# Kernel tuning notes

Measured on AMD Instinct MI355X. Metric: run time of the kernel, lower is better.

## Reference

```python
import jax, jax.numpy as jnp
import numpy as np

MS0 = 4            # base sector size (ms[0])
MS1 = 4            # top sector size (r=[1] -> ms[-1]=ms0)
Q = 2              # q_length (Ising spin states)
C = 512            # c_length
LAYERS = 2
B = 256
L = 16
FS = MS0 * MS0 - 1  # neighborhood size, excludes target pixel


def setup_inputs():
    key = jax.random.key(0)
    ks = jax.random.split(key, 8)
    v = jax.random.randint(ks[0], (B, L, L), 0, Q, dtype=jnp.int32)
    u = v.astype(jnp.float32)
    emb = jax.random.normal(ks[1], (FS, Q, C), dtype=jnp.float32)  # fs embedding tables

    def lin_w(k, out_d, in_d):
        b = 1.0 / np.sqrt(in_d)
        return jax.random.uniform(k, (out_d, in_d), minval=-b, maxval=b, dtype=jnp.float32)

    def lin_b(k, out_d, in_d):
        b = 1.0 / np.sqrt(in_d)
        return jax.random.uniform(k, (out_d,), minval=-b, maxval=b, dtype=jnp.float32)

    k2a, k2b = jax.random.split(ks[2])
    k3a, k3b = jax.random.split(ks[3])
    mlp_w1 = lin_w(k2a, C, C)
    mlp_b1 = lin_b(k2b, C, C)
    mlp_w2 = lin_w(k3a, Q, C)
    mlp_b2 = lin_b(k3b, Q, C)

    def lstm_p(k, in_d):
        k1, k2, k3, k4 = jax.random.split(k, 4)
        b = 1.0 / np.sqrt(C)
        wi = jax.random.uniform(k1, (4 * C, in_d), minval=-b, maxval=b, dtype=jnp.float32)
        wh = jax.random.uniform(k2, (4 * C, C), minval=-b, maxval=b, dtype=jnp.float32)
        bi = jax.random.uniform(k3, (4 * C,), minval=-b, maxval=b, dtype=jnp.float32)
        bh = jax.random.uniform(k4, (4 * C,), minval=-b, maxval=b, dtype=jnp.float32)
        return wi, wh, bi, bh

    w_ih0, w_hh0, b_ih0, b_hh0 = lstm_p(ks[4], MS1 * MS1)
    w_ih1, w_hh1, b_ih1, b_hh1 = lstm_p(ks[5], C)
    return dict(u=u, v=v, emb=emb,
                mlp_w1=mlp_w1, mlp_b1=mlp_b1, mlp_w2=mlp_w2, mlp_b2=mlp_b2,
                w_ih0=w_ih0, w_hh0=w_hh0, b_ih0=b_ih0, b_hh0=b_hh0,
                w_ih1=w_ih1, w_hh1=w_hh1, b_ih1=b_ih1, b_hh1=b_hh1)


def _forward(u, v, emb, mlp_w1, mlp_b1, mlp_w2, mlp_b2,
             w_ih0, w_hh0, b_ih0, b_hh0, w_ih1, w_hh1, b_ih1, b_hh1):
    n_sec = L // MS0
    margin = MS0 - 1
    lstm_params = ((w_ih0, w_hh0, b_ih0, b_hh0), (w_ih1, w_hh1, b_ih1, b_hh1))

    def lstm_step(x, state):
        # single-timestep multi-layer LSTM (eval mode, no dropout)
        h, c = state  # [LAYERS, B, C] each
        hs, cs = [], []
        inp = x
        for l, (wi, wh, bi, bh) in enumerate(lstm_params):
            g = inp @ wi.T + bi + h[l] @ wh.T + bh
            gi, gf, gg, go = jnp.split(g, 4, axis=-1)  # torch gate order i,f,g,o
            cn = jax.nn.sigmoid(gf) * c[l] + jax.nn.sigmoid(gi) * jnp.tanh(gg)
            hn = jax.nn.sigmoid(go) * jnp.tanh(cn)
            hs.append(hn)
            cs.append(cn)
            inp = hn
        return (jnp.stack(hs), jnp.stack(cs))

    zeros_state = lambda: (jnp.zeros((LAYERS, B, C), jnp.float32),
                           jnp.zeros((LAYERS, B, C), jnp.float32))
    memi = [zeros_state() for _ in range(n_sec)]
    memj = [zeros_state() for _ in range(n_sec)]
    sector = [0, 0]
    softout = jnp.zeros((B, L, L, Q), jnp.float32)
    nbr = jnp.arange(FS)[None, :]  # [1, FS] embedding-table indices
    key = jax.random.key(1234)

    for i in range(n_sec - 1):
        for j in range(n_sec - 1):
            si, sj = i * MS0, j * MS0
            ns0, ns1 = MS1 * (si // MS1), MS1 * (sj // MS1)
            if ns1 != sector[1]:
                sector = [ns0, ns1]
                for s in range(n_sec):
                    uv = u[:, s * MS1:(s + 1) * MS1, sector[1]:sector[1] + MS1].reshape(B, MS1 * MS1)
                    memj[s] = lstm_step(uv, memj[s])
            if ns0 != sector[0]:
                sector[0] = ns0
                uv = u[:, sector[0] - MS1:sector[0], sector[1]:sector[1] + MS1].reshape(B, MS1 * MS1)
                memi[sector[0] // MS1] = lstm_step(uv, memi[sector[0] // MS1])
            h0 = memj[i][0][0] + memi[j][0][0]  # layer-0 hidden sum, [B, C]
            for ii in range(MS0):
                for jj in range(MS0):
                    a, b = si + ii + 1, sj + jj + 1
                    pr, pc = a + margin, b + margin  # target pixel (bottom-right of patch)
                    patch = v[:, a:a + MS0, b:b + MS0].reshape(B, MS0 * MS0)[:, :FS]  # mask drops (margin,margin)
                    xemb = emb[nbr, patch, :].sum(axis=1)  # [B, C]
                    z = jax.nn.relu((xemb + h0) @ mlp_w1.T + mlp_b1)
                    logits = jax.nn.log_softmax(z @ mlp_w2.T + mlp_b2, axis=-1)  # [B, Q]
                    softout = softout.at[:, pr, pc].set(logits)
                    key, sub = jax.random.split(key)
                    samp = jax.random.categorical(sub, logits, axis=-1)  # [B]
                    v = v.at[:, pr, pc].set(samp.astype(v.dtype))
                    u = u.at[:, pr, pc].set(samp.astype(u.dtype))
    return softout, u, v


def reference(u, v, emb, mlp_w1, mlp_b1, mlp_w2, mlp_b2,
              w_ih0, w_hh0, b_ih0, b_hh0, w_ih1, w_hh1, b_ih1, b_hh1):
    return _forward(u, v, emb, mlp_w1, mlp_b1, mlp_w2, mlp_b2,
                    w_ih0, w_hh0, b_ih0, b_hh0, w_ih1, w_hh1, b_ih1, b_hh1)
```

## Files before the change

kernel.cpp:

```cpp
#include <hip/hip_runtime.h>
#include <cstdint>
#include <cstddef>

constexpr int NB = 256;
constexpr int NC = 512;
constexpr int NL = 16;
constexpr int NFS = 15;

#define PARTITIONABLE 1

struct TFOut { uint32_t a, b; };

__host__ __device__ constexpr uint32_t rotl32(uint32_t x, int d) {
  return (x << d) | (x >> (32 - d));
}

__host__ __device__ constexpr TFOut tf2x32(uint32_t k0, uint32_t k1,
                                           uint32_t x0, uint32_t x1) {
  uint32_t k2 = k0 ^ k1 ^ 0x1BD11BDAu;
  x0 += k0; x1 += k1;
  const int R0[4] = {13, 15, 26, 6};
  const int R1[4] = {17, 29, 16, 24};
  for (int i = 0; i < 4; i++) { x0 += x1; x1 = rotl32(x1, R0[i]); x1 ^= x0; }
  x0 += k1; x1 += k2 + 1u;
  for (int i = 0; i < 4; i++) { x0 += x1; x1 = rotl32(x1, R1[i]); x1 ^= x0; }
  x0 += k2; x1 += k0 + 2u;
  for (int i = 0; i < 4; i++) { x0 += x1; x1 = rotl32(x1, R0[i]); x1 ^= x0; }
  x0 += k0; x1 += k1 + 3u;
  for (int i = 0; i < 4; i++) { x0 += x1; x1 = rotl32(x1, R1[i]); x1 ^= x0; }
  x0 += k1; x1 += k2 + 4u;
  for (int i = 0; i < 4; i++) { x0 += x1; x1 = rotl32(x1, R0[i]); x1 ^= x0; }
  x0 += k2; x1 += k0 + 5u;
  return TFOut{x0, x1};
}

struct SubKeys { uint32_t v[288]; };

constexpr SubKeys make_subkeys() {
  SubKeys s{};
  uint32_t k0 = 0u, k1 = 1234u;
  for (int t = 0; t < 144; t++) {
#if PARTITIONABLE
    TFOut nk = tf2x32(k0, k1, 0u, 0u);
    TFOut sk = tf2x32(k0, k1, 0u, 1u);
    s.v[2 * t] = sk.a; s.v[2 * t + 1] = sk.b;
    k0 = nk.a; k1 = nk.b;
#else
    TFOut p0 = tf2x32(k0, k1, 0u, 2u);
    TFOut p1 = tf2x32(k0, k1, 1u, 3u);
    s.v[2 * t] = p0.b; s.v[2 * t + 1] = p1.b;
    k0 = p0.a; k1 = p1.a;
#endif
  }
  return s;
}

__constant__ SubKeys SUBKEYS = make_subkeys();

__device__ __forceinline__ float gumbel_from_bits(uint32_t bits) {
  uint32_t ub = (bits >> 9) | 0x3f800000u;
  float f = __uint_as_float(ub) - 1.0f;
  float u = (f == 0.0f) ? 1.17549435e-38f : f;
  float inner = logf(u);
  float outer = logf(-inner);
  return -outer;
}

typedef __attribute__((ext_vector_type(8))) short bf16x8;
typedef __attribute__((ext_vector_type(4))) float f32x4;

__device__ __forceinline__ void gl2lds16(const unsigned short* g,
                                         unsigned short* l) {
  __builtin_amdgcn_global_load_lds(
      (const __attribute__((address_space(1))) unsigned int*)g,
      (__attribute__((address_space(3))) unsigned int*)l, 16, 0, 0);
}

__device__ __forceinline__ uint32_t bf_rne(float x) {
  uint32_t u = __float_as_uint(x);
  return (u + 0x7fffu + ((u >> 16) & 1u)) >> 16;
}

__global__ __launch_bounds__(256) void setup_kernel(
    const float* __restrict__ u_in, const int* __restrict__ v_in,
    float* __restrict__ h0buf, float* __restrict__ cbuf,
    float* __restrict__ u_cur, int* __restrict__ v_cur,
    float* __restrict__ out_soft, float* __restrict__ out_u,
    float* __restrict__ out_v, unsigned int* __restrict__ az) {
  int idx = blockIdx.x * 256 + threadIdx.x;
  if (idx < 786432) h0buf[idx] = 0.0f;
  if (idx < 3 * NB * NC) cbuf[idx] = 0.0f;
  if (idx < 786432) az[idx] = 0u;
  if (idx < NB * NL * NL) {
    float uv = u_in[idx];
    int vv = v_in[idx];
    u_cur[idx] = uv;
    v_cur[idx] = vv;
    out_u[idx] = uv;
    out_v[idx] = (float)vv;
  }
  if (idx < NB * NL * NL * 2) out_soft[idx] = 0.0f;
}

__global__ __launch_bounds__(256) void split_w_kernel(
    const float* __restrict__ whh,
    unsigned short* __restrict__ Bhi, unsigned short* __restrict__ Blo) {
  int idx = blockIdx.x * 256 + threadIdx.x;
  float x = whh[idx];
  uint32_t hb = bf_rne(x);
  float lo = x - __uint_as_float(hb << 16);
  Bhi[idx] = (unsigned short)hb;
  Blo[idx] = (unsigned short)bf_rne(lo);
}

__global__ __launch_bounds__(256) void wd_kernel(
    const float* __restrict__ emb, const float* __restrict__ w1,
    const float* __restrict__ b1, float* __restrict__ WD,
    float* __restrict__ A0v) {
  __shared__ double dvec[NC];
  int n = blockIdx.x, tid = threadIdx.x;
  for (int k = tid; k < NC; k += 256) {
    if (n < NFS) {
      dvec[k] = (double)emb[(n * 2 + 1) * NC + k] - (double)emb[(n * 2) * NC + k];
    } else {
      double s = 0.0;
      for (int nn = 0; nn < NFS; nn++) s += (double)emb[(nn * 2) * NC + k];
      dvec[k] = s;
    }
  }
  __syncthreads();
  for (int c = tid; c < NC; c += 256) {
    double acc = 0.0;
    const float* wrow = w1 + (size_t)c * NC;
    for (int k = 0; k < NC; k++) acc += dvec[k] * (double)wrow[k];
    if (n < NFS) WD[n * NC + c] = (float)acc;
    else         A0v[c] = (float)(acc + (double)b1[c]);
  }
}

__global__ __launch_bounds__(256) void lstm_fused2_kernel(
    const unsigned short* __restrict__ Ah_r, const unsigned short* __restrict__ Al_r,
    unsigned short* __restrict__ Ah_w, unsigned short* __restrict__ Al_w,
    const unsigned short* __restrict__ Bhi, const unsigned short* __restrict__ Blo,
    const float* __restrict__ wih, const float* __restrict__ u_cur,
    const float* __restrict__ bih, const float* __restrict__ bhh,
    float* __restrict__ cbuf, float* __restrict__ h_out, int col0) {
  __shared__ __align__(16) unsigned short SM[24576];
  __shared__ float uvs[32][16];

  unsigned short* sA  = SM;
  unsigned short* sAl = SM + 4096;
  unsigned short* sB  = SM + 8192;
  unsigned short* sBl = SM + 16384;

  int bx0 = blockIdx.x;
  int xcd = bx0 & 7;
  int i5 = bx0 >> 3;
  int ct = xcd * 4 + (i5 & 3);
  int rt = i5 >> 2;
  int tid = threadIdx.x;
  int w = tid >> 6, lane = tid & 63;
  int l15 = lane & 15, kg = lane >> 4;
  int sw = (l15 >> 1) & 3;
  int grow0 = rt * 32;
  int s = rt >> 3;
  int b0 = (rt & 7) * 32;

  {
    int idx = tid;
    for (int t = 0; t < 2; t++, idx += 256) {
      int r = idx >> 4, nn = idx & 15;
      uvs[r][nn] =
          u_cur[(b0 + r) * 256 + (s * 4 + (nn >> 2)) * 16 + col0 + (nn & 3)];
    }
  }

  f32x4 acc[2][4];
#pragma unroll
  for (int i = 0; i < 2; i++)
#pragma unroll
    for (int j = 0; j < 4; j++) acc[i][j] = (f32x4){0.f, 0.f, 0.f, 0.f};

  for (int kc = 0; kc < 4; kc++) {
    int k0 = w * 128 + kc * 32;
    if (kc > 0) __syncthreads();
#pragma unroll
    for (int q = 0; q < 2; q++) {
      int slot = q * 64 + lane;
      int r = slot >> 2;
      int c2 = (slot & 3) ^ ((r >> 1) & 3);
      size_t so = (size_t)(grow0 + r) * 512 + k0 + c2 * 8;
      gl2lds16(Ah_r + so, sA + w * 1024 + q * 512);
      gl2lds16(Al_r + so, sAl + w * 1024 + q * 512);
    }
#pragma unroll
    for (int q = 0; q < 4; q++) {
      int slot = q * 64 + lane;
      int r = slot >> 2;
      int c2 = (slot & 3) ^ ((r >> 1) & 3);
      int nidx = (r >> 4) * 512 + ct * 16 + (r & 15);
      size_t so = (size_t)nidx * 512 + k0 + c2 * 8;
      gl2lds16(Bhi + so, sB + w * 2048 + q * 512);
      gl2lds16(Blo + so, sBl + w * 2048 + q * 512);
    }
    __syncthreads();

    bf16x8 ah[2], al[2];
#pragma unroll
    for (int i = 0; i < 2; i++) {
      int ro = w * 1024 + (i * 16 + l15) * 32 + ((kg ^ sw) * 8);
      ah[i] = *(const bf16x8*)&sA[ro];
      al[i] = *(const bf16x8*)&sAl[ro];
    }
#pragma unroll
    for (int j = 0; j < 4; j++) {
      int ro = w * 2048 + (j * 16 + l15) * 32 + ((kg ^ sw) * 8);
      bf16x8 bh = *(const bf16x8*)&sB[ro];
      bf16x8 bl = *(const bf16x8*)&sBl[ro];
#pragma unroll
      for (int i = 0; i < 2; i++) {
        acc[i][j] = __builtin_amdgcn_mfma_f32_16x16x32_bf16(ah[i], bh,
                                                            acc[i][j], 0, 0, 0);
        acc[i][j] = __builtin_amdgcn_mfma_f32_16x16x32_bf16(ah[i], bl,
                                                            acc[i][j], 0, 0, 0);
        acc[i][j] = __builtin_amdgcn_mfma_f32_16x16x32_bf16(al[i], bh,
                                                            acc[i][j], 0, 0, 0);
      }
    }
  }

  float* red = (float*)SM;
  __syncthreads();
#pragma unroll
  for (int i = 0; i < 2; i++)
#pragma unroll
    for (int g = 0; g < 4; g++)
#pragma unroll
      for (int rr = 0; rr < 4; rr++) {
        int row = i * 16 + kg * 4 + rr;
        red[((w * 4 + g) * 32 + row) * 17 + l15] = acc[i][g][rr];
      }
  __syncthreads();

  int rbase = tid >> 4, c = tid & 15;
  int cglob = ct * 16 + c;
  float bi_[4], bh_[4];
#pragma unroll
  for (int g = 0; g < 4; g++) {
    bi_[g] = bih[g * 512 + cglob];
    bh_[g] = bhh[g * 512 + cglob];
  }
#pragma unroll
  for (int rh = 0; rh < 2; rh++) {
    int row = rh * 16 + rbase;
    int grow = grow0 + row;
    float uvr[16];
#pragma unroll
    for (int nn = 0; nn < 16; nn++) uvr[nn] = uvs[row][nn];
    float gv[4];
#pragma unroll
    for (int g = 0; g < 4; g++) {
      float v = 0.0f;
#pragma unroll
      for (int ww = 0; ww < 4; ww++)
        v += red[((ww * 4 + g) * 32 + row) * 17 + c];
      const float* wr = wih + (size_t)(g * 512 + cglob) * 16;
#pragma unroll
      for (int nn = 0; nn < 16; nn++) v = fmaf(uvr[nn], wr[nn], v);
      gv[g] = v + bi_[g] + bh_[g];
    }
    size_t off = (size_t)grow * NC + cglob;
    float c_old = cbuf[off];
    float sig_i = 1.0f / (1.0f + expf(-gv[0]));
    float sig_f = 1.0f / (1.0f + expf(-gv[1]));
    float tg    = tanhf(gv[2]);
    float sig_o = 1.0f / (1.0f + expf(-gv[3]));
    float cn = sig_f * c_old + sig_i * tg;
    float hn = sig_o * tanhf(cn);
    cbuf[off] = cn;
    h_out[off] = hn;
    uint32_t hb = bf_rne(hn);
    float lo = hn - __uint_as_float(hb << 16);
    Ah_w[off] = (unsigned short)hb;
    Al_w[off] = (unsigned short)bf_rne(lo);
  }
}

__global__ __launch_bounds__(256) void w1h0_kernel(
    const float* __restrict__ h_in,
    const float* __restrict__ w1, float* __restrict__ Hpart) {
  int bx = blockIdx.x;
  int ks = bx >> 5;
  int bt = (bx >> 3) & 3;
  int ct = bx & 7;
  int tid = threadIdx.x, tn = tid & 15, tb = tid >> 4;

  __shared__ float hs[64][36];
  __shared__ float wt[64][36];
  float acc[4][4] = {};
  const float* hbase = h_in + (size_t)(bt * 64) * NC;

  for (int kc = 0; kc < 2; kc++) {
    int k0 = ks * 64 + kc * 32;
    __syncthreads();
    for (int t = 0; t < 2; t++) {
      int idx = tid + t * 256;
      int row = idx >> 3, kk4 = idx & 7;
      *(float4*)&hs[row][kk4 * 4] =
          *(const float4*)(hbase + (size_t)row * NC + k0 + kk4 * 4);
      int wrow = ct * 64 + row;
      *(float4*)&wt[row][kk4 * 4] =
          *(const float4*)(w1 + (size_t)wrow * NC + k0 + kk4 * 4);
    }
    __syncthreads();
#pragma unroll
    for (int kk4 = 0; kk4 < 8; kk4++) {
      float4 hv[4], wv[4];
#pragma unroll
      for (int i = 0; i < 4; i++) hv[i] = *(float4*)&hs[tb * 4 + i][kk4 * 4];
#pragma unroll
      for (int j = 0; j < 4; j++) wv[j] = *(float4*)&wt[tn + 16 * j][kk4 * 4];
#pragma unroll
      for (int i = 0; i < 4; i++)
#pragma unroll
        for (int j = 0; j < 4; j++)
          acc[i][j] += hv[i].x * wv[j].x + hv[i].y * wv[j].y +
                       hv[i].z * wv[j].z + hv[i].w * wv[j].w;
    }
  }
#pragma unroll
  for (int i = 0; i < 4; i++) {
    int b = bt * 64 + tb * 4 + i;
#pragma unroll
    for (int j = 0; j < 4; j++) {
      int cidx = ct * 64 + tn + 16 * j;
      Hpart[((size_t)ks * NB + b) * NC + cidx] = acc[i][j];
    }
  }
}

__global__ __launch_bounds__(64) void pixel_kernel(
    const float* __restrict__ WD, const float* __restrict__ A0v,
    const float* __restrict__ Hpart, const float* __restrict__ w2,
    const float* __restrict__ b2, float* __restrict__ u_cur,
    int* __restrict__ v_cur, float* __restrict__ out_soft,
    float* __restrict__ out_u, float* __restrict__ out_v,
    int si, int sj, int t_base) {
  int b = blockIdx.x, lane = threadIdx.x;
  __shared__ float gum[32];

  int widx = (lane < 49) ? lane : 48;
  int vv = v_cur[b * 256 + (si + 1 + widx / 7) * 16 + (sj + 1 + widx % 7)];
  unsigned long long mask = __ballot((lane < 49) && (vv != 0));

  if (lane < 32) {
    int t = t_base + (lane >> 1);
    uint32_t sk0 = SUBKEYS.v[2 * t], sk1 = SUBKEYS.v[2 * t + 1];
    uint32_t bits;
#if PARTITIONABLE
    TFOut o = tf2x32(sk0, sk1, 0u, (uint32_t)(2 * b + (lane & 1)));
    bits = o.a ^ o.b;
#else
    uint32_t f = (uint32_t)(2 * b + (lane & 1));
    if (f < 256u) { TFOut o = tf2x32(sk0, sk1, f, f + 256u); bits = o.a; }
    else          { TFOut o = tf2x32(sk0, sk1, f - 256u, f); bits = o.b; }
#endif
    gum[lane] = gumbel_from_bits(bits);
  }

  float wdreg[NFS][8];
#pragma unroll
  for (int n = 0; n < NFS; n++)
#pragma unroll
    for (int r = 0; r < 8; r++) wdreg[n][r] = WD[n * NC + lane + 64 * r];

  float w2r0[8], w2r1[8];
#pragma unroll
  for (int r = 0; r < 8; r++) {
    w2r0[r] = w2[lane + 64 * r];
    w2r1[r] = w2[NC + lane + 64 * r];
  }
  double b20 = (double)b2[0], b21 = (double)b2[1];

  float base[8];
#pragma unroll
  for (int r = 0; r < 8; r++) {
    int c = lane + 64 * r;
    float v = A0v[c];
#pragma unroll
    for (int ks = 0; ks < 8; ks++) v += Hpart[((size_t)ks * NB + b) * NC + c];
    base[r] = v;
  }
  __syncthreads();

#pragma unroll 1
  for (int ii = 0; ii < 4; ii++) {
#pragma unroll 1
    for (int jj = 0; jj < 4; jj++) {
      int bofs = ii * 7 + jj;
      float acc[8];
#pragma unroll
      for (int r = 0; r < 8; r++) acc[r] = base[r];
#pragma unroll
      for (int n = 0; n < NFS; n++) {
        const int OFF = (n / 4) * 7 + (n % 4);
        float pf = (float)((unsigned)((mask >> (bofs + OFF)) & 1ull));
#pragma unroll
        for (int r = 0; r < 8; r++) acc[r] = fmaf(pf, wdreg[n][r], acc[r]);
      }
      double d0 = 0.0, d1 = 0.0;
#pragma unroll
      for (int r = 0; r < 8; r++) {
        float z = fmaxf(acc[r], 0.0f);
        d0 += (double)z * (double)w2r0[r];
        d1 += (double)z * (double)w2r1[r];
      }
#pragma unroll
      for (int off = 32; off > 0; off >>= 1) {
        d0 += __shfl_xor(d0, off, 64);
        d1 += __shfl_xor(d1, off, 64);
      }
      float r0 = (float)(d0 + b20);
      float r1 = (float)(d1 + b21);
      float m = fmaxf(r0, r1);
      float s0 = r0 - m, s1 = r1 - m;
      float lse = logf(expf(s0) + expf(s1));
      float l0 = s0 - lse, l1 = s1 - lse;
      int pidx = ii * 4 + jj;
      float a0 = l0 + gum[2 * pidx];
      float a1 = l1 + gum[2 * pidx + 1];
      int samp = (a1 > a0) ? 1 : 0;
      int tbit = bofs + 24;
      mask = (mask & ~(1ull << tbit)) | ((unsigned long long)samp << tbit);
      if (lane == 0) {
        int pr = si + ii + 4, pc = sj + jj + 4;
        size_t so = ((size_t)(b * 16 + pr) * 16 + pc) * 2;
        out_soft[so] = l0;
        out_soft[so + 1] = l1;
        int po = b * 256 + pr * 16 + pc;
        float fs = (float)samp;
        u_cur[po] = fs;
        v_cur[po] = samp;
        out_u[po] = fs;
        out_v[po] = fs;
      }
    }
  }
}

extern "C" void kernel_launch(void* const* d_in, const int* in_sizes, int n_in,
                              void* d_out, int out_size, void* d_ws,
                              size_t ws_size, hipStream_t stream) {
  (void)in_sizes; (void)n_in; (void)out_size; (void)ws_size;
  const float* u_in = (const float*)d_in[0];
  const int*   v_in = (const int*)d_in[1];
  const float* emb  = (const float*)d_in[2];
  const float* w1   = (const float*)d_in[3];
  const float* b1   = (const float*)d_in[4];
  const float* w2   = (const float*)d_in[5];
  const float* b2   = (const float*)d_in[6];
  const float* wih  = (const float*)d_in[7];
  const float* whh  = (const float*)d_in[8];
  const float* bih  = (const float*)d_in[9];
  const float* bhh  = (const float*)d_in[10];

  float* ws = (float*)d_ws;
  const size_t HP = (size_t)3 * NB * NC;
  float* h0buf = ws;
  float* cbuf  = h0buf + 2 * HP;
  float* Hpart = cbuf + (size_t)3 * NB * NC;
  float* WDp   = Hpart + (size_t)8 * NB * NC;
  float* A0v   = WDp + NFS * NC;
  float* u_cur = A0v + NC;
  int*   v_cur = (int*)(u_cur + NB * NL * NL);
  unsigned short* Ahi = (unsigned short*)(v_cur + NB * NL * NL);
  unsigned short* Alo = Ahi + (size_t)2 * 768 * 512;
  unsigned short* Bhi = Alo + (size_t)2 * 768 * 512;
  unsigned short* Blo = Bhi + (size_t)2048 * 512;
  const size_t APAR = (size_t)768 * 512;

  float* out_soft = (float*)d_out;
  float* out_u = out_soft + NB * NL * NL * 2;
  float* out_v = out_u + NB * NL * NL;

  setup_kernel<<<dim3(4096), dim3(256), 0, stream>>>(
      u_in, v_in, h0buf, cbuf, u_cur, v_cur, out_soft, out_u, out_v,
      (unsigned int*)Ahi);
  split_w_kernel<<<dim3(4096), dim3(256), 0, stream>>>(whh, Bhi, Blo);
  wd_kernel<<<dim3(16), dim3(256), 0, stream>>>(emb, w1, b1, WDp, A0v);

  for (int k = 0; k < 9; k++) {
    if (k > 0) {
      int e = k - 1;
      int col0 = (e % 3 == 0) ? 4 : ((e % 3 == 1) ? 8 : 0);
      int rp = e & 1, wp = rp ^ 1;
      lstm_fused2_kernel<<<dim3(768), dim3(256), 0, stream>>>(
          Ahi + (size_t)rp * APAR, Alo + (size_t)rp * APAR,
          Ahi + (size_t)wp * APAR, Alo + (size_t)wp * APAR,
          Bhi, Blo, wih, u_cur, bih, bhh, cbuf,
          h0buf + (size_t)wp * HP, col0);
    }
    w1h0_kernel<<<dim3(256), dim3(256), 0, stream>>>(
        h0buf + (size_t)(k & 1) * HP + (size_t)(k / 3) * NB * NC, w1, Hpart);
    pixel_kernel<<<dim3(256), dim3(64), 0, stream>>>(
        WDp, A0v, Hpart, w2, b2, u_cur, v_cur, out_soft, out_u, out_v,
        (k / 3) * 4, (k % 3) * 4, k * 16);
  }
}
```

Measured before the change: 485.1 us.

## Prefetch next K-slice in LSTM MFMA loop and split w1h0 into more partials

The LSTM fused kernel now issues the global-to-LDS loads for the next K-chunk right after reading the current chunk into registers, using waitcnt and sched barriers instead of block-wide syncs. This overlaps memory latency with the MFMA work. Separately, the w1h0 GEMM splits K into 16 partials of 32 instead of 8 of 64, doubling the grid to 512 blocks. The pixel kernel now sums 16 partials and the workspace layout grows to match. The prefetch writes the same per-wave LDS region that was just read, so correctness relies on the lgkmcnt wait covering those reads. The extra partials add more reduction reads.

```diff
diff --git a/kernel.cpp b/kernel.cpp
--- a/kernel.cpp
+++ b/kernel.cpp
@@ -181,9 +181,7 @@
 #pragma unroll
     for (int j = 0; j < 4; j++) acc[i][j] = (f32x4){0.f, 0.f, 0.f, 0.f};
 
-  for (int kc = 0; kc < 4; kc++) {
-    int k0 = w * 128 + kc * 32;
-    if (kc > 0) __syncthreads();
+  auto STAGE = [&](int k0) {
 #pragma unroll
     for (int q = 0; q < 2; q++) {
       int slot = q * 64 + lane;
@@ -203,9 +201,15 @@
       gl2lds16(Bhi + so, sB + w * 2048 + q * 512);
       gl2lds16(Blo + so, sBl + w * 2048 + q * 512);
     }
-    __syncthreads();
-
-    bf16x8 ah[2], al[2];
+  };
+
+  STAGE(w * 128);
+
+  for (int kc = 0; kc < 4; kc++) {
+    asm volatile("s_waitcnt vmcnt(0)" ::: "memory");
+    __builtin_amdgcn_sched_barrier(0);
+
+    bf16x8 ah[2], al[2], bh[4], bl[4];
 #pragma unroll
     for (int i = 0; i < 2; i++) {
       int ro = w * 1024 + (i * 16 + l15) * 32 + ((kg ^ sw) * 8);
@@ -215,18 +219,26 @@
 #pragma unroll
     for (int j = 0; j < 4; j++) {
       int ro = w * 2048 + (j * 16 + l15) * 32 + ((kg ^ sw) * 8);
-      bf16x8 bh = *(const bf16x8*)&sB[ro];
-      bf16x8 bl = *(const bf16x8*)&sBl[ro];
+      bh[j] = *(const bf16x8*)&sB[ro];
+      bl[j] = *(const bf16x8*)&sBl[ro];
+    }
+    asm volatile("s_waitcnt lgkmcnt(0)" ::: "memory");
+    __builtin_amdgcn_sched_barrier(0);
+
+    if (kc < 3) STAGE(w * 128 + (kc + 1) * 32);
+    __builtin_amdgcn_sched_barrier(0);
+
+#pragma unroll
+    for (int j = 0; j < 4; j++)
 #pragma unroll
       for (int i = 0; i < 2; i++) {
-        acc[i][j] = __builtin_amdgcn_mfma_f32_16x16x32_bf16(ah[i], bh,
+        acc[i][j] = __builtin_amdgcn_mfma_f32_16x16x32_bf16(ah[i], bh[j],
                                                             acc[i][j], 0, 0, 0);
-        acc[i][j] = __builtin_amdgcn_mfma_f32_16x16x32_bf16(ah[i], bl,
+        acc[i][j] = __builtin_amdgcn_mfma_f32_16x16x32_bf16(ah[i], bl[j],
                                                             acc[i][j], 0, 0, 0);
-        acc[i][j] = __builtin_amdgcn_mfma_f32_16x16x32_bf16(al[i], bh,
+        acc[i][j] = __builtin_amdgcn_mfma_f32_16x16x32_bf16(al[i], bh[j],
                                                             acc[i][j], 0, 0, 0);
       }
-    }
   }
 
   float* red = (float*)SM;
@@ -299,34 +311,31 @@
   __shared__ float wt[64][36];
   float acc[4][4] = {};
   const float* hbase = h_in + (size_t)(bt * 64) * NC;
-
-  for (int kc = 0; kc < 2; kc++) {
-    int k0 = ks * 64 + kc * 32;
-    __syncthreads();
-    for (int t = 0; t < 2; t++) {
-      int idx = tid + t * 256;
-      int row = idx >> 3, kk4 = idx & 7;
-      *(float4*)&hs[row][kk4 * 4] =
-          *(const float4*)(hbase + (size_t)row * NC + k0 + kk4 * 4);
-      int wrow = ct * 64 + row;
-      *(float4*)&wt[row][kk4 * 4] =
-          *(const float4*)(w1 + (size_t)wrow * NC + k0 + kk4 * 4);
-    }
-    __syncthreads();
-#pragma unroll
-    for (int kk4 = 0; kk4 < 8; kk4++) {
-      float4 hv[4], wv[4];
-#pragma unroll
-      for (int i = 0; i < 4; i++) hv[i] = *(float4*)&hs[tb * 4 + i][kk4 * 4];
-#pragma unroll
-      for (int j = 0; j < 4; j++) wv[j] = *(float4*)&wt[tn + 16 * j][kk4 * 4];
-#pragma unroll
-      for (int i = 0; i < 4; i++)
-#pragma unroll
-        for (int j = 0; j < 4; j++)
-          acc[i][j] += hv[i].x * wv[j].x + hv[i].y * wv[j].y +
-                       hv[i].z * wv[j].z + hv[i].w * wv[j].w;
-    }
+  int k0 = ks * 32;
+
+  for (int t = 0; t < 2; t++) {
+    int idx = tid + t * 256;
+    int row = idx >> 3, kk4 = idx & 7;
+    *(float4*)&hs[row][kk4 * 4] =
+        *(const float4*)(hbase + (size_t)row * NC + k0 + kk4 * 4);
+    int wrow = ct * 64 + row;
+    *(float4*)&wt[row][kk4 * 4] =
+        *(const float4*)(w1 + (size_t)wrow * NC + k0 + kk4 * 4);
+  }
+  __syncthreads();
+#pragma unroll
+  for (int kk4 = 0; kk4 < 8; kk4++) {
+    float4 hv[4], wv[4];
+#pragma unroll
+    for (int i = 0; i < 4; i++) hv[i] = *(float4*)&hs[tb * 4 + i][kk4 * 4];
+#pragma unroll
+    for (int j = 0; j < 4; j++) wv[j] = *(float4*)&wt[tn + 16 * j][kk4 * 4];
+#pragma unroll
+    for (int i = 0; i < 4; i++)
+#pragma unroll
+      for (int j = 0; j < 4; j++)
+        acc[i][j] += hv[i].x * wv[j].x + hv[i].y * wv[j].y +
+                     hv[i].z * wv[j].z + hv[i].w * wv[j].w;
   }
 #pragma unroll
   for (int i = 0; i < 4; i++) {
@@ -388,7 +397,7 @@
     int c = lane + 64 * r;
     float v = A0v[c];
 #pragma unroll
-    for (int ks = 0; ks < 8; ks++) v += Hpart[((size_t)ks * NB + b) * NC + c];
+    for (int ks = 0; ks < 16; ks++) v += Hpart[((size_t)ks * NB + b) * NC + c];
     base[r] = v;
   }
   __syncthreads();
@@ -469,7 +478,7 @@
   float* h0buf = ws;
   float* cbuf  = h0buf + 2 * HP;
   float* Hpart = cbuf + (size_t)3 * NB * NC;
-  float* WDp   = Hpart + (size_t)8 * NB * NC;
+  float* WDp   = Hpart + (size_t)16 * NB * NC;
   float* A0v   = WDp + NFS * NC;
   float* u_cur = A0v + NC;
   int*   v_cur = (int*)(u_cur + NB * NL * NL);
@@ -500,7 +509,7 @@
           Bhi, Blo, wih, u_cur, bih, bhh, cbuf,
           h0buf + (size_t)wp * HP, col0);
     }
-    w1h0_kernel<<<dim3(256), dim3(256), 0, stream>>>(
+    w1h0_kernel<<<dim3(512), dim3(256), 0, stream>>>(
         h0buf + (size_t)(k & 1) * HP + (size_t)(k / 3) * NB * NC, w1, Hpart);
     pixel_kernel<<<dim3(256), dim3(64), 0, stream>>>(
         WDp, A0v, Hpart, w2, b2, u_cur, v_cur, out_soft, out_u, out_v,
```

Result: no change. 491.8 us (+1.4%).
